# Kernel tuning notes

Measured on AMD Instinct MI355X. Metric: run time of the kernel, lower is better.

## Reference

```python
import jax, jax.numpy as jnp
import numpy as np

N_EDGES = 1_250_000
N_NODES = 100_000
EDGE_DIM = 64
N_RADIAL = 16
OUT_DIM = 1


def setup_inputs() -> dict:
    key = jax.random.key(0)
    ks = jax.random.split(key, 12)
    s_e = 1.0 / np.sqrt(EDGE_DIM)
    s_r = 1.0 / np.sqrt(N_RADIAL)
    return {
        "x": jax.random.normal(ks[0], (N_EDGES, EDGE_DIM), jnp.float32),
        "rbf": jax.random.uniform(ks[1], (N_EDGES, N_RADIAL), jnp.float32),
        "idx_i": jax.random.randint(ks[2], (N_EDGES,), 0, N_NODES, jnp.int64),
        "num_nodes": N_NODES,
        # rbf_dense: Dense(n_radial, edge_dim, bias=False) -> weight (edge_dim, n_radial)
        "W_rbf": jax.random.normal(ks[3], (EDGE_DIM, N_RADIAL), jnp.float32) * s_r,
        # three hidden Dense(edge_dim, edge_dim) with bias
        "W1": jax.random.normal(ks[4], (EDGE_DIM, EDGE_DIM), jnp.float32) * s_e,
        "b1": jnp.zeros((EDGE_DIM,), jnp.float32),
        "W2": jax.random.normal(ks[5], (EDGE_DIM, EDGE_DIM), jnp.float32) * s_e,
        "b2": jnp.zeros((EDGE_DIM,), jnp.float32),
        "W3": jax.random.normal(ks[6], (EDGE_DIM, EDGE_DIM), jnp.float32) * s_e,
        "b3": jnp.zeros((EDGE_DIM,), jnp.float32),
        # final Dense(edge_dim, out_dim, bias=False) -> weight (out_dim, edge_dim)
        "W_out": jax.random.normal(ks[7], (OUT_DIM, EDGE_DIM), jnp.float32) * s_e,
    }


def swish(h):
    # Swish(beta=1.0): h * sigmoid(h)
    return h * jax.nn.sigmoid(h)


def reference(x, rbf, idx_i, num_nodes, W_rbf, W1, b1, W2, b2, W3, b3, W_out):
    # edge gating: Dense(rbf) * x  -> (n_edge, edge_dim)
    e = (rbf @ W_rbf.T) * x
    # scatter-add edges to center nodes -> (n_node, edge_dim)
    h = jax.ops.segment_sum(e, idx_i, num_segments=num_nodes)
    h = swish(h @ W1.T + b1)
    h = swish(h @ W2.T + b2)
    h = swish(h @ W3.T + b3)
    return h @ W_out.T
```

## Files before the change

### kernel.cpp

```cpp
#include <hip/hip_runtime.h>
#include <cstdint>



__global__ __launch_bounds__(256) void k_hist(
    const int* __restrict__ idx, int* __restrict__ counts, int n_edges)
{
    const int i = blockIdx.x * blockDim.x + threadIdx.x;
    const int stride = gridDim.x * blockDim.x;
    for (int e = i; e < n_edges; e += stride)
        atomicAdd(&counts[idx[e]], 1);
}

__global__ __launch_bounds__(256) void k_scan1(
    const int* __restrict__ counts, int* __restrict__ offsets,
    int* __restrict__ blocksum, int n_nodes)
{
    __shared__ int sh[256];
    const int t = threadIdx.x;
    const int i = blockIdx.x * 256 + t;
    const int v = (i < n_nodes) ? counts[i] : 0;
    sh[t] = v;
    __syncthreads();
    for (int off = 1; off < 256; off <<= 1) {
        const int add = (t >= off) ? sh[t - off] : 0;
        __syncthreads();
        sh[t] += add;
        __syncthreads();
    }
    if (i < n_nodes) offsets[i] = sh[t] - v;
    if (t == 255) blocksum[blockIdx.x] = sh[255];
}

__global__ __launch_bounds__(512) void k_scan2(int* __restrict__ blocksum, int nb)
{
    __shared__ int sh[512];
    const int t = threadIdx.x;
    const int v = (t < nb) ? blocksum[t] : 0;
    sh[t] = v;
    __syncthreads();
    for (int off = 1; off < 512; off <<= 1) {
        const int add = (t >= off) ? sh[t - off] : 0;
        __syncthreads();
        sh[t] += add;
        __syncthreads();
    }
    if (t < nb) blocksum[t] = sh[t] - v;
}

__global__ __launch_bounds__(256) void k_addbase(
    int* __restrict__ offsets, const int* __restrict__ blocksum,
    int* __restrict__ cursor, int n_nodes, int n_edges)
{
    const int i = blockIdx.x * 256 + threadIdx.x;
    if (i < n_nodes) {
        const int o = offsets[i] + blocksum[blockIdx.x];
        offsets[i] = o;
        cursor[i]  = o;
    }
    if (i == 0) offsets[n_nodes] = n_edges;
}

__global__ __launch_bounds__(256) void k_scatter(
    const int* __restrict__ idx, int* __restrict__ cursor,
    int* __restrict__ perm, int n_edges)
{
    const int i = blockIdx.x * blockDim.x + threadIdx.x;
    const int stride = gridDim.x * blockDim.x;
    for (int e = i; e < n_edges; e += stride) {
        const int pos = atomicAdd(&cursor[idx[e]], 1);
        perm[pos] = e;
    }
}

__global__ __launch_bounds__(256) void k_gather(
    const float* __restrict__ x,
    const float* __restrict__ rbf,
    const int*   __restrict__ offsets,
    const int*   __restrict__ perm,
    const float* __restrict__ Wrbf,
    float* __restrict__ hacc,
    int n_nodes)
{
    const int lane = threadIdx.x & 63;
    const int n    = blockIdx.x * (blockDim.x >> 6) + (threadIdx.x >> 6);
    if (n >= n_nodes) return;

    float w[16];
    {
        const float4* wp = (const float4*)(Wrbf + (size_t)lane * 16);
        float4 a = wp[0], b = wp[1], c = wp[2], d = wp[3];
        w[0]=a.x; w[1]=a.y; w[2]=a.z; w[3]=a.w;
        w[4]=b.x; w[5]=b.y; w[6]=b.z; w[7]=b.w;
        w[8]=c.x; w[9]=c.y; w[10]=c.z; w[11]=c.w;
        w[12]=d.x; w[13]=d.y; w[14]=d.z; w[15]=d.w;
    }

    const int s     = offsets[n];
    const int e_end = offsets[n + 1];

    float acc = 0.0f;
    int e = (s < e_end) ? perm[s] : 0;
    for (int j = s; j < e_end; ++j) {
        const int e_nxt = (j + 1 < e_end) ? perm[j + 1] : 0;

        const float4* rp = (const float4*)(rbf + (size_t)e * 16);
        float4 r0 = rp[0], r1 = rp[1], r2 = rp[2], r3 = rp[3];
        const float xv = x[(size_t)e * 64 + lane];

        float g = 0.0f;
        g = fmaf(r0.x, w[0],  g); g = fmaf(r0.y, w[1],  g);
        g = fmaf(r0.z, w[2],  g); g = fmaf(r0.w, w[3],  g);
        g = fmaf(r1.x, w[4],  g); g = fmaf(r1.y, w[5],  g);
        g = fmaf(r1.z, w[6],  g); g = fmaf(r1.w, w[7],  g);
        g = fmaf(r2.x, w[8],  g); g = fmaf(r2.y, w[9],  g);
        g = fmaf(r2.z, w[10], g); g = fmaf(r2.w, w[11], g);
        g = fmaf(r3.x, w[12], g); g = fmaf(r3.y, w[13], g);
        g = fmaf(r3.z, w[14], g); g = fmaf(r3.w, w[15], g);

        acc = fmaf(g, xv, acc);
        e = e_nxt;
    }
    hacc[(size_t)n * 64 + lane] = acc;
}

__global__ __launch_bounds__(256) void edge_kernel(
    const float* __restrict__ x, const float* __restrict__ rbf,
    const int* __restrict__ idx, const float* __restrict__ Wrbf,
    float* __restrict__ hacc, int n_edges, int n_nodes)
{
    const int lane   = threadIdx.x & 63;
    const int wave   = blockIdx.x * (blockDim.x >> 6) + (threadIdx.x >> 6);
    const int nwaves = gridDim.x * (blockDim.x >> 6);

    float w[16];
    {
        const float4* wp = (const float4*)(Wrbf + (size_t)lane * 16);
        float4 a = wp[0], b = wp[1], c = wp[2], d = wp[3];
        w[0]=a.x; w[1]=a.y; w[2]=a.z; w[3]=a.w;
        w[4]=b.x; w[5]=b.y; w[6]=b.z; w[7]=b.w;
        w[8]=c.x; w[9]=c.y; w[10]=c.z; w[11]=c.w;
        w[12]=d.x; w[13]=d.y; w[14]=d.z; w[15]=d.w;
    }

    for (int e = wave; e < n_edges; e += nwaves) {
        const int node = idx[e];
        const float4* rp = (const float4*)(rbf + (size_t)e * 16);
        float4 r0 = rp[0], r1 = rp[1], r2 = rp[2], r3 = rp[3];
        float rv[16] = { r0.x, r0.y, r0.z, r0.w, r1.x, r1.y, r1.z, r1.w,
                         r2.x, r2.y, r2.z, r2.w, r3.x, r3.y, r3.z, r3.w };
        float g = 0.0f;
#pragma unroll
        for (int r = 0; r < 16; ++r) g = fmaf(rv[r], w[r], g);
        const float xv = x[(size_t)e * 64 + lane];
        if ((unsigned)node < (unsigned)n_nodes)
            atomicAdd(&hacc[(size_t)node * 64 + lane], g * xv);
    }
}

__device__ __forceinline__ void gemm_tile(
    const float (*__restrict__ Hin)[68], const float* __restrict__ Wg,
    int n0, int d0, float acc[4][4])
{
#pragma unroll
    for (int i = 0; i < 4; ++i)
#pragma unroll
        for (int j = 0; j < 4; ++j) acc[i][j] = 0.0f;

#pragma unroll 2
    for (int k4 = 0; k4 < 16; ++k4) {
        float4 h4[4], w4[4];
#pragma unroll
        for (int i = 0; i < 4; ++i)
            h4[i] = *(const float4*)(&Hin[n0 + i][k4 * 4]);
#pragma unroll
        for (int j = 0; j < 4; ++j)
            w4[j] = *(const float4*)(Wg + (size_t)(d0 + j) * 64 + k4 * 4);
#pragma unroll
        for (int i = 0; i < 4; ++i)
#pragma unroll
            for (int j = 0; j < 4; ++j) {
                acc[i][j] = fmaf(h4[i].x, w4[j].x, acc[i][j]);
                acc[i][j] = fmaf(h4[i].y, w4[j].y, acc[i][j]);
                acc[i][j] = fmaf(h4[i].z, w4[j].z, acc[i][j]);
                acc[i][j] = fmaf(h4[i].w, w4[j].w, acc[i][j]);
            }
    }
}

__device__ __forceinline__ float swish_f(float v)
{
    return v / (1.0f + __expf(-v));
}

__global__ __launch_bounds__(256) void node_gemm(
    const float* __restrict__ hacc,
    const float* __restrict__ W1, const float* __restrict__ b1,
    const float* __restrict__ W2, const float* __restrict__ b2,
    const float* __restrict__ W3, const float* __restrict__ b3,
    const float* __restrict__ Wout,
    float* __restrict__ out, int n_nodes)
{
    __shared__ float Ha[64][68];
    __shared__ float Hb[64][68];
    __shared__ float bsh[3][64];
    __shared__ float wosh[64];

    const int t    = threadIdx.x;
    const int base = blockIdx.x * 64;

    if (t < 64) {
        bsh[0][t] = b1[t];
        bsh[1][t] = b2[t];
        bsh[2][t] = b3[t];
        wosh[t]   = Wout[t];
    }

    {
        const int tc = t & 15;
        const int r0 = t >> 4;
#pragma unroll
        for (int rr = 0; rr < 4; ++rr) {
            const int r    = r0 + rr * 16;
            const int node = base + r;
            float4 v = make_float4(0.f, 0.f, 0.f, 0.f);
            if (node < n_nodes)
                v = *(const float4*)(hacc + (size_t)node * 64 + tc * 4);
            *(float4*)(&Ha[r][tc * 4]) = v;
        }
    }
    __syncthreads();

    const int lane = t & 63;
    const int w    = t >> 6;
    const int td   = lane & 15;
    const int tn   = (lane >> 4) + (w << 2);
    const int d0   = td * 4;
    const int n0   = tn * 4;

    float acc[4][4];

    gemm_tile(Ha, W1, n0, d0, acc);
#pragma unroll
    for (int i = 0; i < 4; ++i) {
        float4 o;
        o.x = swish_f(acc[i][0] + bsh[0][d0 + 0]);
        o.y = swish_f(acc[i][1] + bsh[0][d0 + 1]);
        o.z = swish_f(acc[i][2] + bsh[0][d0 + 2]);
        o.w = swish_f(acc[i][3] + bsh[0][d0 + 3]);
        *(float4*)(&Hb[n0 + i][d0]) = o;
    }
    __syncthreads();

    gemm_tile(Hb, W2, n0, d0, acc);
#pragma unroll
    for (int i = 0; i < 4; ++i) {
        float4 o;
        o.x = swish_f(acc[i][0] + bsh[1][d0 + 0]);
        o.y = swish_f(acc[i][1] + bsh[1][d0 + 1]);
        o.z = swish_f(acc[i][2] + bsh[1][d0 + 2]);
        o.w = swish_f(acc[i][3] + bsh[1][d0 + 3]);
        *(float4*)(&Ha[n0 + i][d0]) = o;
    }
    __syncthreads();

    gemm_tile(Ha, W3, n0, d0, acc);
    float p[4];
#pragma unroll
    for (int i = 0; i < 4; ++i) {
        float s = 0.0f;
        s = fmaf(swish_f(acc[i][0] + bsh[2][d0 + 0]), wosh[d0 + 0], s);
        s = fmaf(swish_f(acc[i][1] + bsh[2][d0 + 1]), wosh[d0 + 1], s);
        s = fmaf(swish_f(acc[i][2] + bsh[2][d0 + 2]), wosh[d0 + 2], s);
        s = fmaf(swish_f(acc[i][3] + bsh[2][d0 + 3]), wosh[d0 + 3], s);
        p[i] = s;
    }
#pragma unroll
    for (int i = 0; i < 4; ++i) {
        p[i] += __shfl_xor(p[i], 8, 64);
        p[i] += __shfl_xor(p[i], 4, 64);
        p[i] += __shfl_xor(p[i], 2, 64);
        p[i] += __shfl_xor(p[i], 1, 64);
    }
    if (td == 0) {
#pragma unroll
        for (int i = 0; i < 4; ++i) {
            const int node = base + n0 + i;
            if (node < n_nodes) out[node] = p[i];
        }
    }
}

extern "C" void kernel_launch(void* const* d_in, const int* in_sizes, int n_in,
                              void* d_out, int out_size, void* d_ws, size_t ws_size,
                              hipStream_t stream)
{
    const float* x    = (const float*)d_in[0];
    const float* rbf  = (const float*)d_in[1];
    const int*   idx  = (const int*)d_in[2];
    const float* Wrbf = (const float*)d_in[4];
    const float* W1   = (const float*)d_in[5];
    const float* b1   = (const float*)d_in[6];
    const float* W2   = (const float*)d_in[7];
    const float* b2   = (const float*)d_in[8];
    const float* W3   = (const float*)d_in[9];
    const float* b3   = (const float*)d_in[10];
    const float* Wout = (const float*)d_in[11];

    const int n_edges = in_sizes[0] / 64;
    const int n_nodes = out_size;

    const size_t N_pad = ((size_t)n_nodes + 1 + 63) & ~(size_t)63;
    const size_t E_pad = ((size_t)n_edges + 63) & ~(size_t)63;
    int*   counts = (int*)d_ws;
    int*   offs   = counts + N_pad;
    int*   bsum   = offs + N_pad;
    int*   perm   = bsum + 512;
    float* hacc   = (float*)(perm + E_pad);

    const size_t need = (2 * N_pad + 512 + E_pad) * sizeof(int)
                      + (size_t)n_nodes * 64 * sizeof(float);

    const int NB = (n_nodes + 255) / 256;

    if (ws_size >= need && NB <= 512) {
        hipMemsetAsync(counts, 0, (size_t)n_nodes * sizeof(int), stream);
        k_hist   <<<2048, 256, 0, stream>>>(idx, counts, n_edges);
        k_scan1  <<<NB,   256, 0, stream>>>(counts, offs, bsum, n_nodes);
        k_scan2  <<<1,    512, 0, stream>>>(bsum, NB);
        k_addbase<<<NB,   256, 0, stream>>>(offs, bsum, counts, n_nodes, n_edges);
        k_scatter<<<2048, 256, 0, stream>>>(idx, counts, perm, n_edges);

        const int gblocks = (n_nodes + 3) / 4;
        k_gather<<<gblocks, 256, 0, stream>>>(x, rbf, offs, perm, Wrbf,
                                              hacc, n_nodes);
    } else {
        hacc = (float*)d_ws;
        hipMemsetAsync(hacc, 0, (size_t)n_nodes * 64 * sizeof(float), stream);
        edge_kernel<<<8192, 256, 0, stream>>>(x, rbf, idx, Wrbf, hacc,
                                              n_edges, n_nodes);
    }

    const int mlp_blocks = (n_nodes + 63) / 64;
    node_gemm<<<mlp_blocks, 256, 0, stream>>>(hacc, W1, b1, W2, b2, W3, b3,
                                              Wout, (float*)d_out, n_nodes);
}
```

Before: 983.3 us.

## Reassociate gather to accumulate rbf outer x then apply W_rbf once per node

The gather kernel now accumulates a per-lane 16-entry sum of rbf[e][r]*x[e][lane] over a node's edges and multiplies by the W_rbf row once at the end, instead of computing the gate dot product for every edge. Edge indices and segment bounds are made wave-uniform with readfirstlane so rbf loads can become scalar loads. The main loop is unrolled by four with prefetch of the next perm entries to expose more memory parallelism. The cost is 16 extra accumulator registers and a changed floating-point summation order.

```diff
diff --git a/kernel.cpp b/kernel.cpp
--- a/kernel.cpp
+++ b/kernel.cpp
@@ -71,6 +71,21 @@
         const int pos = atomicAdd(&cursor[idx[e]], 1);
         perm[pos] = e;
     }
+}
+
+__device__ __forceinline__ void rbf_accum(
+    const float* __restrict__ rbf, int e, float xv, float M[16])
+{
+    const float4* rp = (const float4*)(rbf + (size_t)e * 16);
+    float4 r0 = rp[0], r1 = rp[1], r2 = rp[2], r3 = rp[3];
+    M[0]  = fmaf(r0.x, xv, M[0]);  M[1]  = fmaf(r0.y, xv, M[1]);
+    M[2]  = fmaf(r0.z, xv, M[2]);  M[3]  = fmaf(r0.w, xv, M[3]);
+    M[4]  = fmaf(r1.x, xv, M[4]);  M[5]  = fmaf(r1.y, xv, M[5]);
+    M[6]  = fmaf(r1.z, xv, M[6]);  M[7]  = fmaf(r1.w, xv, M[7]);
+    M[8]  = fmaf(r2.x, xv, M[8]);  M[9]  = fmaf(r2.y, xv, M[9]);
+    M[10] = fmaf(r2.z, xv, M[10]); M[11] = fmaf(r2.w, xv, M[11]);
+    M[12] = fmaf(r3.x, xv, M[12]); M[13] = fmaf(r3.y, xv, M[13]);
+    M[14] = fmaf(r3.z, xv, M[14]); M[15] = fmaf(r3.w, xv, M[15]);
 }
 
 __global__ __launch_bounds__(256) void k_gather(
@@ -83,7 +98,8 @@
     int n_nodes)
 {
     const int lane = threadIdx.x & 63;
-    const int n    = blockIdx.x * (blockDim.x >> 6) + (threadIdx.x >> 6);
+    int n = blockIdx.x * (blockDim.x >> 6) + (threadIdx.x >> 6);
+    n = __builtin_amdgcn_readfirstlane(n);
     if (n >= n_nodes) return;
 
     float w[16];
@@ -96,31 +112,53 @@
         w[12]=d.x; w[13]=d.y; w[14]=d.z; w[15]=d.w;
     }
 
-    const int s     = offsets[n];
-    const int e_end = offsets[n + 1];
+    const int s     = __builtin_amdgcn_readfirstlane(offsets[n]);
+    const int e_end = __builtin_amdgcn_readfirstlane(offsets[n + 1]);
+
+    float M[16];
+#pragma unroll
+    for (int r = 0; r < 16; ++r) M[r] = 0.0f;
+
+    int j = s;
+    const int cnt = e_end - s;
+
+    const int rem = cnt & 3;
+    for (int k = 0; k < rem; ++k, ++j) {
+        const int e = __builtin_amdgcn_readfirstlane(perm[j]);
+        const float xv = x[(size_t)e * 64 + lane];
+        rbf_accum(rbf, e, xv, M);
+    }
+
+    if (j < e_end) {
+        int e0 = __builtin_amdgcn_readfirstlane(perm[j + 0]);
+        int e1 = __builtin_amdgcn_readfirstlane(perm[j + 1]);
+        int e2 = __builtin_amdgcn_readfirstlane(perm[j + 2]);
+        int e3 = __builtin_amdgcn_readfirstlane(perm[j + 3]);
+        while (j < e_end) {
+            const float xv0 = x[(size_t)e0 * 64 + lane];
+            const float xv1 = x[(size_t)e1 * 64 + lane];
+            const float xv2 = x[(size_t)e2 * 64 + lane];
+            const float xv3 = x[(size_t)e3 * 64 + lane];
+            const int c0 = e0, c1 = e1, c2 = e2, c3 = e3;
+
+            j += 4;
+            if (j < e_end) {
+                e0 = __builtin_amdgcn_readfirstlane(perm[j + 0]);
+                e1 = __builtin_amdgcn_readfirstlane(perm[j + 1]);
+                e2 = __builtin_amdgcn_readfirstlane(perm[j + 2]);
+                e3 = __builtin_amdgcn_readfirstlane(perm[j + 3]);
+            }
+
+            rbf_accum(rbf, c0, xv0, M);
+            rbf_accum(rbf, c1, xv1, M);
+            rbf_accum(rbf, c2, xv2, M);
+            rbf_accum(rbf, c3, xv3, M);
+        }
+    }
 
     float acc = 0.0f;
-    int e = (s < e_end) ? perm[s] : 0;
-    for (int j = s; j < e_end; ++j) {
-        const int e_nxt = (j + 1 < e_end) ? perm[j + 1] : 0;
-
-        const float4* rp = (const float4*)(rbf + (size_t)e * 16);
-        float4 r0 = rp[0], r1 = rp[1], r2 = rp[2], r3 = rp[3];
-        const float xv = x[(size_t)e * 64 + lane];
-
-        float g = 0.0f;
-        g = fmaf(r0.x, w[0],  g); g = fmaf(r0.y, w[1],  g);
-        g = fmaf(r0.z, w[2],  g); g = fmaf(r0.w, w[3],  g);
-        g = fmaf(r1.x, w[4],  g); g = fmaf(r1.y, w[5],  g);
-        g = fmaf(r1.z, w[6],  g); g = fmaf(r1.w, w[7],  g);
-        g = fmaf(r2.x, w[8],  g); g = fmaf(r2.y, w[9],  g);
-        g = fmaf(r2.z, w[10], g); g = fmaf(r2.w, w[11], g);
-        g = fmaf(r3.x, w[12], g); g = fmaf(r3.y, w[13], g);
-        g = fmaf(r3.z, w[14], g); g = fmaf(r3.w, w[15], g);
-
-        acc = fmaf(g, xv, acc);
-        e = e_nxt;
-    }
+#pragma unroll
+    for (int r = 0; r < 16; ++r) acc = fmaf(w[r], M[r], acc);
     hacc[(size_t)n * 64 + lane] = acc;
 }
 
```

Result: faster. 848.7 us (-13.7%).
